# Optimization experiments

Measured on AMD Instinct MI355X. Metric: run time of the kernel, lower is better.

## Reference

```python
import jax, jax.numpy as jnp
import numpy as np

NEG_SLOPE = 0.2  # PyG GATConv default negative_slope


def setup_inputs() -> dict:
    key = jax.random.key(0)
    k_x, k_e, k_w, k_as, k_ad = jax.random.split(key, 5)
    B, F, N, D, E, L = 2, 16, 5000, 128, 40000, 3
    x = jax.random.normal(k_x, (B, F, N, D), dtype=jnp.float32)
    edge_index = jax.random.randint(k_e, (B, F, 2, E), 0, N, dtype=jnp.int64)
    Ws = jax.random.normal(k_w, (L, D, D), dtype=jnp.float32) / np.float32(np.sqrt(D))
    att_src = jax.random.normal(k_as, (L, D), dtype=jnp.float32) / np.float32(np.sqrt(D))
    att_dst = jax.random.normal(k_ad, (L, D), dtype=jnp.float32) / np.float32(np.sqrt(D))
    bias = jnp.zeros((L, D), dtype=jnp.float32)
    return {"x": x, "edge_index": edge_index, "Ws": Ws,
            "att_src": att_src, "att_dst": att_dst, "bias": bias}


def _gat_layer(h, src, dst, n, W, a_s, a_d, b):
    # h: [n, D] node features; src/dst: [E_tot] edge endpoints (self-loops included)
    h2 = h @ W                                   # [n, D] transformed features
    s = h2 @ a_s                                 # [n] per-node source score
    d = h2 @ a_d                                 # [n] per-node dest score
    e = jax.nn.leaky_relu(s[src] + d[dst], NEG_SLOPE)   # [E_tot] raw attention
    m = jax.lax.stop_gradient(jax.ops.segment_max(e, dst, num_segments=n))
    ex = jnp.exp(e - m[dst])                     # numerically stable softmax per dst
    denom = jax.ops.segment_sum(ex, dst, num_segments=n)
    alpha = ex / denom[dst]                      # [E_tot] normalized attention
    out = jax.ops.segment_sum(alpha[:, None] * h2[src], dst, num_segments=n) + b
    return jax.nn.relu(out)


def reference(x, edge_index, Ws, att_src, att_dst, bias):
    B, F, N, D = x.shape
    n = B * F * N
    h = x.reshape(n, D)
    # faithful to torch: (BF,2,E).view(2,-1) is a raw row-major reshape
    ei = edge_index.reshape(2, -1)
    loop = jnp.arange(n, dtype=ei.dtype)         # PyG GATConv adds self-loops
    src = jnp.concatenate([ei[0], loop])
    dst = jnp.concatenate([ei[1], loop])
    for l in range(Ws.shape[0]):                 # fixed small layer loop
        h = _gat_layer(h, src, dst, n, Ws[l], att_src[l], att_dst[l], bias[l])
    return h.reshape(B, F, N, D)
```

## Files before the change

### kernel.cpp

```cpp
#include <hip/hip_runtime.h>
#include <math.h>

#define NODES_TOTAL 160000
#define NODES_REAL  5000
#define D 128
#define NEG 0.2f
#define KP2 128
#define HL2 (128 * KP2)
#define WT2_L (2 * HL2)

typedef unsigned short ushort_t;
typedef unsigned int uint_t;
typedef __attribute__((ext_vector_type(8))) __bf16 bf16x8;
typedef __attribute__((ext_vector_type(4))) float f32x4;
union BF8 { bf16x8 v; ushort_t u[8]; };

__device__ __forceinline__ void split2(float x, ushort_t& hi, ushort_t& lo) {
    unsigned u = __float_as_uint(x);
    hi = (ushort_t)(u >> 16);
    float hif = __uint_as_float(u & 0xffff0000u);
    lo = (ushort_t)(__float_as_uint(x - hif) >> 16);
}
__device__ __forceinline__ uint_t encmax(float f) {
    uint_t b = __float_as_uint(f);
    return b ^ ((uint_t)((int)b >> 31) | 0x80000000u);
}
__device__ __forceinline__ float decmax(uint_t u) {
    uint_t b = (u & 0x80000000u) ? (u ^ 0x80000000u) : ~u;
    return __uint_as_float(b);
}

__global__ void zero_kernel(int* counts, uint_t* gmaxu) {
    int i = blockIdx.x * blockDim.x + threadIdx.x;
    if (i < NODES_REAL) counts[i] = 0;
    if (i < 3) gmaxu[i] = 0u;
}

__global__ void rank_kernel(const int* __restrict__ ei, int* __restrict__ counts,
                            ushort_t* __restrict__ rank16, int Eh) {
    int e = blockIdx.x * blockDim.x + threadIdx.x;
    if (e < Eh) {
        int d = ei[Eh + e];
        int r = atomicAdd(&counts[d], 1);
        rank16[e] = (ushort_t)r;
    }
}

__global__ void scan_kernel(const int* __restrict__ counts, int* __restrict__ offs) {
    __shared__ int sd[1024];
    int t = threadIdx.x;
    int pre[5]; int sum = 0;
    #pragma unroll
    for (int u = 0; u < 5; ++u) {
        int idx = t * 5 + u;
        int c = (idx < NODES_REAL) ? counts[idx] : 0;
        pre[u] = sum; sum += c;
    }
    sd[t] = sum;
    __syncthreads();
    int run = sum;
    for (int o = 1; o < 1024; o <<= 1) {
        int v = (t >= o) ? sd[t - o] : 0;
        __syncthreads();
        sd[t] += v;
        __syncthreads();
    }
    int excl = sd[t] - run;
    #pragma unroll
    for (int u = 0; u < 5; ++u) {
        int idx = t * 5 + u;
        if (idx < NODES_REAL) offs[idx] = excl + pre[u];
    }
    if (t == 1023) offs[NODES_REAL] = excl + run;
}

__global__ void scatter_det(const int* __restrict__ ei, const int* __restrict__ offs,
                            const ushort_t* __restrict__ rank16, ushort_t* __restrict__ esrc,
                            int Eh) {
    int e = blockIdx.x * blockDim.x + threadIdx.x;
    if (e < Eh) {
        int s = ei[e];
        int d = ei[Eh + e];
        esrc[offs[d] + (int)rank16[e]] = (ushort_t)s;
    }
}

__global__ void wsplit_kernel(const float* __restrict__ Ws, ushort_t* __restrict__ Wm) {
    int l  = blockIdx.x >> 3;
    int n  = (blockIdx.x & 7) * 16 + (threadIdx.x >> 4);
    int c8 = threadIdx.x & 15;
    int k0 = c8 * 8;
    const float* src = Ws + (size_t)l * D * D;
    union { ushort_t u[8]; uint4 v; } hi, lo;
    #pragma unroll
    for (int j = 0; j < 8; ++j) split2(src[(size_t)(k0 + j) * D + n], hi.u[j], lo.u[j]);
    int ct = n >> 4, m16 = n & 15, kc = c8 >> 2, qq = c8 & 3;
    int lane = qq * 16 + m16;
    ushort_t* d2 = Wm + (size_t)l * WT2_L + ((ct * 4 + kc) * 2 + 0) * 512 + lane * 8;
    *(uint4*)d2 = hi.v;
    *(uint4*)(d2 + 512) = lo.v;
}

__global__ __launch_bounds__(256, 2)
void mlp3_kernel(const float* __restrict__ x, const ushort_t* __restrict__ Wm,
                 const float* __restrict__ bs, float* __restrict__ out, int row_base) {
    __shared__ float scr[2][2][16][132];
    int tid = threadIdx.x;
    int w = tid >> 6, lane = tid & 63, q = lane >> 4, m16 = lane & 15;
    int p = w >> 1, h = w & 1;
    int row0 = row_base + blockIdx.x * 64 + p * 32;

    float4 xa[2][4][2];
    #pragma unroll
    for (int rt = 0; rt < 2; ++rt) {
        int r = row0 + rt * 16 + m16;
        if (r > NODES_TOTAL - 1) r = NODES_TOTAL - 1;
        #pragma unroll
        for (int kc = 0; kc < 4; ++kc) {
            const float* gp = x + (size_t)r * D + kc * 32 + q * 8;
            xa[rt][kc][0] = *(const float4*)gp;
            xa[rt][kc][1] = *(const float4*)(gp + 4);
        }
    }

    f32x4 acc[2][4];
    #pragma unroll
    for (int l = 0; l < 3; ++l) {
        const ushort_t* Wml = Wm + (size_t)l * WT2_L;
        if (l > 0) __syncthreads();

        BF8 ahi[2][4], alo[2][4];
        #pragma unroll
        for (int rt = 0; rt < 2; ++rt)
            #pragma unroll
            for (int kc = 0; kc < 4; ++kc) {
                float4 v0, v1;
                if (l == 0) { v0 = xa[rt][kc][0]; v1 = xa[rt][kc][1]; }
                else {
                    const float* sp = &scr[p][rt][m16][kc * 32 + q * 8];
                    v0 = *(const float4*)sp; v1 = *(const float4*)(sp + 4);
                }
                float xv[8] = {v0.x, v0.y, v0.z, v0.w, v1.x, v1.y, v1.z, v1.w};
                #pragma unroll
                for (int j = 0; j < 8; ++j) split2(xv[j], ahi[rt][kc].u[j], alo[rt][kc].u[j]);
            }
        if (l > 0) __syncthreads();

        #pragma unroll
        for (int rt = 0; rt < 2; ++rt)
            #pragma unroll
            for (int ct = 0; ct < 4; ++ct) acc[rt][ct] = (f32x4){0.f, 0.f, 0.f, 0.f};

        #pragma unroll
        for (int ph = 0; ph < 2; ++ph) {
            int kc0 = ph * 2;
            bf16x8 bh[4][2], bl[4][2];
            #pragma unroll
            for (int ct = 0; ct < 4; ++ct)
                #pragma unroll
                for (int dk = 0; dk < 2; ++dk) {
                    const ushort_t* bp = Wml + (((h * 4 + ct) * 4 + (kc0 + dk)) * 2) * 512 + lane * 8;
                    bh[ct][dk] = *(const bf16x8*)bp;
                    bl[ct][dk] = *(const bf16x8*)(bp + 512);
                }
            #pragma unroll
            for (int dk = 0; dk < 2; ++dk)
                #pragma unroll
                for (int ct = 0; ct < 4; ++ct)
                    #pragma unroll
                    for (int rt = 0; rt < 2; ++rt) {
                        acc[rt][ct] = __builtin_amdgcn_mfma_f32_16x16x32_bf16(ahi[rt][kc0 + dk].v, bh[ct][dk], acc[rt][ct], 0, 0, 0);
                        acc[rt][ct] = __builtin_amdgcn_mfma_f32_16x16x32_bf16(ahi[rt][kc0 + dk].v, bl[ct][dk], acc[rt][ct], 0, 0, 0);
                        acc[rt][ct] = __builtin_amdgcn_mfma_f32_16x16x32_bf16(alo[rt][kc0 + dk].v, bh[ct][dk], acc[rt][ct], 0, 0, 0);
                    }
        }
        float bv[4];
        #pragma unroll
        for (int ct = 0; ct < 4; ++ct) bv[ct] = bs[l * D + (h * 4 + ct) * 16 + m16];
        #pragma unroll
        for (int rt = 0; rt < 2; ++rt)
            #pragma unroll
            for (int ct = 0; ct < 4; ++ct)
                #pragma unroll
                for (int reg = 0; reg < 4; ++reg)
                    scr[p][rt][q * 4 + reg][(h * 4 + ct) * 16 + m16] =
                        fmaxf(acc[rt][ct][reg] + bv[ct], 0.f);
    }
    __syncthreads();
    #pragma unroll
    for (int i = 0; i < 8; ++i) {
        int rowl = i * 2 + (lane >> 5);
        int grow = row0 + h * 16 + rowl;
        float4 v = *(const float4*)&scr[p][h][rowl][(lane & 31) * 4];
        if (grow < NODES_TOTAL)
            *(float4*)&out[(size_t)grow * D + (lane & 31) * 4] = v;
    }
}

__global__ __launch_bounds__(64, 2)
void gsmall_kernel(const float* __restrict__ hin, const ushort_t* __restrict__ Wm,
                   const float* __restrict__ a_s, const float* __restrict__ a_d,
                   float* __restrict__ h2, float* __restrict__ sv, float* __restrict__ dv,
                   uint_t* __restrict__ gmaxu) {
    int lane = threadIdx.x & 63, q = lane >> 4, m16 = lane & 15;
    int row0 = blockIdx.x * 16;
    float4 xa[4][2];
    {
        int r = row0 + m16;
        if (r > NODES_REAL - 1) r = NODES_REAL - 1;
        #pragma unroll
        for (int kc = 0; kc < 4; ++kc) {
            const float* gp = hin + (size_t)r * D + kc * 32 + q * 8;
            xa[kc][0] = *(const float4*)gp;
            xa[kc][1] = *(const float4*)(gp + 4);
        }
    }
    f32x4 acc[8];
    #pragma unroll
    for (int ct = 0; ct < 8; ++ct) acc[ct] = (f32x4){0.f, 0.f, 0.f, 0.f};

    #pragma unroll
    for (int kc = 0; kc < 4; ++kc) {
        BF8 ahi, alo;
        {
            float4 v0 = xa[kc][0], v1 = xa[kc][1];
            float xv[8] = {v0.x, v0.y, v0.z, v0.w, v1.x, v1.y, v1.z, v1.w};
            #pragma unroll
            for (int j = 0; j < 8; ++j) split2(xv[j], ahi.u[j], alo.u[j]);
        }
        bf16x8 bh[8], bl[8];
        #pragma unroll
        for (int ct = 0; ct < 8; ++ct) {
            const ushort_t* bp = Wm + ((ct * 4 + kc) * 2) * 512 + lane * 8;
            bh[ct] = *(const bf16x8*)bp;
            bl[ct] = *(const bf16x8*)(bp + 512);
        }
        #pragma unroll
        for (int ct = 0; ct < 8; ++ct) {
            acc[ct] = __builtin_amdgcn_mfma_f32_16x16x32_bf16(ahi.v, bh[ct], acc[ct], 0, 0, 0);
            acc[ct] = __builtin_amdgcn_mfma_f32_16x16x32_bf16(ahi.v, bl[ct], acc[ct], 0, 0, 0);
            acc[ct] = __builtin_amdgcn_mfma_f32_16x16x32_bf16(alo.v, bh[ct], acc[ct], 0, 0, 0);
        }
    }
    #pragma unroll
    for (int reg = 0; reg < 4; ++reg) {
        int grow = row0 + q * 4 + reg;
        if (grow < NODES_REAL) {
            #pragma unroll
            for (int ct = 0; ct < 8; ++ct)
                h2[(size_t)grow * D + ct * 16 + m16] = acc[ct][reg];
        }
    }
    float asv[8], adv[8];
    #pragma unroll
    for (int ct = 0; ct < 8; ++ct) { asv[ct] = a_s[ct * 16 + m16]; adv[ct] = a_d[ct * 16 + m16]; }
    #pragma unroll
    for (int reg = 0; reg < 4; ++reg) {
        float ps = 0.f, pd = 0.f;
        #pragma unroll
        for (int ct = 0; ct < 8; ++ct) {
            float v = acc[ct][reg];
            ps += v * asv[ct]; pd += v * adv[ct];
        }
        #pragma unroll
        for (int o = 1; o < 16; o <<= 1) { ps += __shfl_xor(ps, o); pd += __shfl_xor(pd, o); }
        int grow = row0 + q * 4 + reg;
        if (m16 == 0 && grow < NODES_REAL) {
            sv[grow] = ps; dv[grow] = pd;
            atomicMax(gmaxu, encmax(ps));
        }
    }
}

__global__ __launch_bounds__(256)
void agg_kernel(const float* __restrict__ h2, const float* __restrict__ sv,
                const float* __restrict__ dv, const int* __restrict__ offs,
                const ushort_t* __restrict__ esrc, const float* __restrict__ bias,
                float* __restrict__ out, const uint_t* __restrict__ gmaxu) {
    int w = threadIdx.x >> 6, lane = threadIdx.x & 63;
    int i = blockIdx.x * 4 + w;
    int start = offs[i], end = offs[i + 1];
    float d_i = dv[i];
    float gm = decmax(*gmaxu) + d_i;
    float m = gm > 0.f ? gm : NEG * gm;
    const float2* h2v = (const float2*)h2;
    float ax0 = 0.f, ay0 = 0.f, ax1 = 0.f, ay1 = 0.f;
    float ax2 = 0.f, ay2 = 0.f, ax3 = 0.f, ay3 = 0.f, exs = 0.f;
    for (int base = start; base < end; base += 64) {
        int cnt = min(64, end - base);
        int srci = (lane < cnt) ? (int)esrc[base + lane] : 0;
        float sc = sv[srci] + d_i;
        sc = sc > 0.f ? sc : NEG * sc;
        float ex = (lane < cnt) ? __expf(sc - m) : 0.f;
        exs += ex;
        if (cnt == 64) {
            #pragma unroll 2
            for (int j = 0; j < 64; j += 4) {
                int   s0 = __shfl(srci, j),     s1 = __shfl(srci, j + 1);
                int   s2 = __shfl(srci, j + 2), s3 = __shfl(srci, j + 3);
                float e0 = __shfl(ex, j),       e1 = __shfl(ex, j + 1);
                float e2 = __shfl(ex, j + 2),   e3 = __shfl(ex, j + 3);
                float2 hv0 = h2v[(size_t)s0 * 64 + lane];
                float2 hv1 = h2v[(size_t)s1 * 64 + lane];
                float2 hv2 = h2v[(size_t)s2 * 64 + lane];
                float2 hv3 = h2v[(size_t)s3 * 64 + lane];
                ax0 += e0 * hv0.x; ay0 += e0 * hv0.y;
                ax1 += e1 * hv1.x; ay1 += e1 * hv1.y;
                ax2 += e2 * hv2.x; ay2 += e2 * hv2.y;
                ax3 += e3 * hv3.x; ay3 += e3 * hv3.y;
            }
        } else {
            for (int j = 0; j < cnt; ++j) {
                int   src = __shfl(srci, j);
                float e   = __shfl(ex, j);
                float2 hv = h2v[(size_t)src * 64 + lane];
                ax0 += e * hv.x; ay0 += e * hv.y;
            }
        }
    }
    float ax = (ax0 + ax1) + (ax2 + ax3);
    float ay = (ay0 + ay1) + (ay2 + ay3);
    float scf = sv[i] + d_i; scf = scf > 0.f ? scf : NEG * scf;
    float exf = __expf(scf - m);
    float2 hv = h2v[(size_t)i * 64 + lane];
    ax += exf * hv.x; ay += exf * hv.y;
    #pragma unroll
    for (int o = 1; o < 64; o <<= 1) exs += __shfl_xor(exs, o);
    float rd = 1.f / (exs + exf);
    float2 b2 = *(const float2*)&bias[2 * lane];
    float2 o2 = make_float2(fmaxf(ax * rd + b2.x, 0.f), fmaxf(ay * rd + b2.y, 0.f));
    *(float2*)&out[(size_t)i * D + 2 * lane] = o2;
}

extern "C" void kernel_launch(void* const* d_in, const int* in_sizes, int n_in,
                              void* d_out, int out_size, void* d_ws, size_t ws_size,
                              hipStream_t stream) {
    const float* x   = (const float*)d_in[0];
    const int*   ei  = (const int*)d_in[1];
    const float* Ws  = (const float*)d_in[2];
    const float* as_ = (const float*)d_in[3];
    const float* ad_ = (const float*)d_in[4];
    const float* bs  = (const float*)d_in[5];
    float* out = (float*)d_out;
    int Eh = in_sizes[1] / 2;

    char* ws = (char*)d_ws;
    float*    h2     = (float*)ws;
    float*    bufS   = (float*)(ws + 2560000);
    float*    sv     = (float*)(ws + 5120000);
    float*    dv     = (float*)(ws + 5140000);
    int*      counts = (int*)  (ws + 5160000);
    int*      offs   = (int*)  (ws + 5180000);
    ushort_t* rank16 = (ushort_t*)(ws + 5200016);
    ushort_t* esrc   = (ushort_t*)(ws + 7760016);
    ushort_t* Wm     = (ushort_t*)(ws + 10320016);
    uint_t*   gmaxu  = (uint_t*)(ws + 10528912);

    zero_kernel<<<(NODES_REAL + 255) / 256, 256, 0, stream>>>(counts, gmaxu);
    rank_kernel<<<(Eh + 255) / 256, 256, 0, stream>>>(ei, counts, rank16, Eh);
    scan_kernel<<<1, 1024, 0, stream>>>(counts, offs);
    scatter_det<<<(Eh + 255) / 256, 256, 0, stream>>>(ei, offs, rank16, esrc, Eh);
    wsplit_kernel<<<24, 256, 0, stream>>>(Ws, Wm);

    {
        const int rows = NODES_TOTAL - NODES_REAL;
        const int nb   = (rows + 63) / 64;
        const int nb1  = (nb + 2) / 3;
        int base = NODES_REAL;
        for (int s = 0; s < 3; ++s) {
            int b0 = s * nb1;
            int bn = (s == 2) ? (nb - 2 * nb1) : nb1;
            if (bn <= 0) break;
            mlp3_kernel<<<bn, 256, 0, stream>>>(x, Wm, bs, out, base + b0 * 64);
        }
    }

    for (int l = 0; l < 3; ++l) {
        const float* hin = (l == 0) ? x : bufS;
        float* hout = (l == 2) ? out : bufS;
        gsmall_kernel<<<(NODES_REAL + 15) / 16, 64, 0, stream>>>(
            hin, Wm + (size_t)l * WT2_L, as_ + l * D, ad_ + l * D, h2, sv, dv, gmaxu + l);
        agg_kernel<<<(NODES_REAL + 3) / 4, 256, 0, stream>>>(
            h2, sv, dv, offs, esrc, bs + l * D, hout, gmaxu + l);
    }
}
```

Baseline: 540.3 us.

## Use block-local shared-memory ranking, fold zeroing into wsplit, merge MLP launches

Edge ranking now counts per chunk with shared-memory atomics, then does one global atomic per touched node per chunk to get chunk bases. This cuts contention on global counter atomics. The zero kernel is folded into wsplit, and the three mlp3 launches become one. The agg inner loop is software-pipelined so gathers for the next group of four are issued before the FMAs for the current group. The chunk bases live in the h2 scratch buffer, which is safe only because h2 is written later, and the chunk order of global atomics makes edge ordering within a node nondeterministic.

```diff
diff --git a/kernel.cpp b/kernel.cpp
--- a/kernel.cpp
+++ b/kernel.cpp
@@ -8,6 +8,7 @@
 #define KP2 128
 #define HL2 (128 * KP2)
 #define WT2_L (2 * HL2)
+#define CHUNK 16384
 
 typedef unsigned short ushort_t;
 typedef unsigned int uint_t;
@@ -30,19 +31,48 @@
     return __uint_as_float(b);
 }
 
-__global__ void zero_kernel(int* counts, uint_t* gmaxu) {
-    int i = blockIdx.x * blockDim.x + threadIdx.x;
-    if (i < NODES_REAL) counts[i] = 0;
-    if (i < 3) gmaxu[i] = 0u;
-}
-
-__global__ void rank_kernel(const int* __restrict__ ei, int* __restrict__ counts,
-                            ushort_t* __restrict__ rank16, int Eh) {
-    int e = blockIdx.x * blockDim.x + threadIdx.x;
-    if (e < Eh) {
-        int d = ei[Eh + e];
-        int r = atomicAdd(&counts[d], 1);
-        rank16[e] = (ushort_t)r;
+__global__ void wsplit_kernel(const float* __restrict__ Ws, ushort_t* __restrict__ Wm,
+                              int* __restrict__ counts, uint_t* __restrict__ gmaxu) {
+    int gid = blockIdx.x * 256 + threadIdx.x;
+    if (gid < NODES_REAL) counts[gid] = 0;
+    if (gid < 3) gmaxu[gid] = 0u;
+    int l  = blockIdx.x >> 3;
+    int n  = (blockIdx.x & 7) * 16 + (threadIdx.x >> 4);
+    int c8 = threadIdx.x & 15;
+    int k0 = c8 * 8;
+    const float* src = Ws + (size_t)l * D * D;
+    union { ushort_t u[8]; uint4 v; } hi, lo;
+    #pragma unroll
+    for (int j = 0; j < 8; ++j) split2(src[(size_t)(k0 + j) * D + n], hi.u[j], lo.u[j]);
+    int ct = n >> 4, m16 = n & 15, kc = c8 >> 2, qq = c8 & 3;
+    int lane = qq * 16 + m16;
+    ushort_t* d2 = Wm + (size_t)l * WT2_L + ((ct * 4 + kc) * 2 + 0) * 512 + lane * 8;
+    *(uint4*)d2 = hi.v;
+    *(uint4*)(d2 + 512) = lo.v;
+}
+
+__global__ __launch_bounds__(256)
+void rank2_kernel(const int* __restrict__ ei, int* __restrict__ counts,
+                  int* __restrict__ bases, ushort_t* __restrict__ rank16, int Eh) {
+    __shared__ uint_t lc[NODES_REAL];
+    int c = blockIdx.x, tid = threadIdx.x;
+    for (int i = tid; i < NODES_REAL; i += 256) lc[i] = 0u;
+    __syncthreads();
+    int e0 = c * CHUNK;
+    #pragma unroll 4
+    for (int k = 0; k < CHUNK / 256; ++k) {
+        int e = e0 + k * 256 + tid;
+        if (e < Eh) {
+            int d = ei[Eh + e];
+            uint_t r = atomicAdd(&lc[d], 1u);
+            rank16[e] = (ushort_t)r;
+        }
+    }
+    __syncthreads();
+    for (int i = tid; i < NODES_REAL; i += 256) {
+        uint_t n = lc[i];
+        if (n > 0u)
+            bases[c * NODES_REAL + i] = atomicAdd(&counts[i], (int)n);
     }
 }
 
@@ -75,40 +105,26 @@
 }
 
 __global__ void scatter_det(const int* __restrict__ ei, const int* __restrict__ offs,
+                            const int* __restrict__ bases,
                             const ushort_t* __restrict__ rank16, ushort_t* __restrict__ esrc,
                             int Eh) {
     int e = blockIdx.x * blockDim.x + threadIdx.x;
     if (e < Eh) {
         int s = ei[e];
         int d = ei[Eh + e];
-        esrc[offs[d] + (int)rank16[e]] = (ushort_t)s;
-    }
-}
-
-__global__ void wsplit_kernel(const float* __restrict__ Ws, ushort_t* __restrict__ Wm) {
-    int l  = blockIdx.x >> 3;
-    int n  = (blockIdx.x & 7) * 16 + (threadIdx.x >> 4);
-    int c8 = threadIdx.x & 15;
-    int k0 = c8 * 8;
-    const float* src = Ws + (size_t)l * D * D;
-    union { ushort_t u[8]; uint4 v; } hi, lo;
-    #pragma unroll
-    for (int j = 0; j < 8; ++j) split2(src[(size_t)(k0 + j) * D + n], hi.u[j], lo.u[j]);
-    int ct = n >> 4, m16 = n & 15, kc = c8 >> 2, qq = c8 & 3;
-    int lane = qq * 16 + m16;
-    ushort_t* d2 = Wm + (size_t)l * WT2_L + ((ct * 4 + kc) * 2 + 0) * 512 + lane * 8;
-    *(uint4*)d2 = hi.v;
-    *(uint4*)(d2 + 512) = lo.v;
+        int c = e >> 14;
+        esrc[offs[d] + bases[c * NODES_REAL + d] + (int)rank16[e]] = (ushort_t)s;
+    }
 }
 
 __global__ __launch_bounds__(256, 2)
 void mlp3_kernel(const float* __restrict__ x, const ushort_t* __restrict__ Wm,
-                 const float* __restrict__ bs, float* __restrict__ out, int row_base) {
+                 const float* __restrict__ bs, float* __restrict__ out) {
     __shared__ float scr[2][2][16][132];
     int tid = threadIdx.x;
     int w = tid >> 6, lane = tid & 63, q = lane >> 4, m16 = lane & 15;
     int p = w >> 1, h = w & 1;
-    int row0 = row_base + blockIdx.x * 64 + p * 32;
+    int row0 = NODES_REAL + blockIdx.x * 64 + p * 32;
 
     float4 xa[2][4][2];
     #pragma unroll
@@ -294,21 +310,30 @@
         float ex = (lane < cnt) ? __expf(sc - m) : 0.f;
         exs += ex;
         if (cnt == 64) {
-            #pragma unroll 2
-            for (int j = 0; j < 64; j += 4) {
-                int   s0 = __shfl(srci, j),     s1 = __shfl(srci, j + 1);
-                int   s2 = __shfl(srci, j + 2), s3 = __shfl(srci, j + 3);
-                float e0 = __shfl(ex, j),       e1 = __shfl(ex, j + 1);
-                float e2 = __shfl(ex, j + 2),   e3 = __shfl(ex, j + 3);
-                float2 hv0 = h2v[(size_t)s0 * 64 + lane];
-                float2 hv1 = h2v[(size_t)s1 * 64 + lane];
-                float2 hv2 = h2v[(size_t)s2 * 64 + lane];
-                float2 hv3 = h2v[(size_t)s3 * 64 + lane];
+            float e0 = __shfl(ex, 0), e1 = __shfl(ex, 1);
+            float e2 = __shfl(ex, 2), e3 = __shfl(ex, 3);
+            float2 hv0 = h2v[(size_t)__shfl(srci, 0) * 64 + lane];
+            float2 hv1 = h2v[(size_t)__shfl(srci, 1) * 64 + lane];
+            float2 hv2 = h2v[(size_t)__shfl(srci, 2) * 64 + lane];
+            float2 hv3 = h2v[(size_t)__shfl(srci, 3) * 64 + lane];
+            for (int j = 4; j < 64; j += 4) {
+                float f0 = __shfl(ex, j),     f1 = __shfl(ex, j + 1);
+                float f2 = __shfl(ex, j + 2), f3 = __shfl(ex, j + 3);
+                float2 nv0 = h2v[(size_t)__shfl(srci, j) * 64 + lane];
+                float2 nv1 = h2v[(size_t)__shfl(srci, j + 1) * 64 + lane];
+                float2 nv2 = h2v[(size_t)__shfl(srci, j + 2) * 64 + lane];
+                float2 nv3 = h2v[(size_t)__shfl(srci, j + 3) * 64 + lane];
                 ax0 += e0 * hv0.x; ay0 += e0 * hv0.y;
                 ax1 += e1 * hv1.x; ay1 += e1 * hv1.y;
                 ax2 += e2 * hv2.x; ay2 += e2 * hv2.y;
                 ax3 += e3 * hv3.x; ay3 += e3 * hv3.y;
+                e0 = f0; e1 = f1; e2 = f2; e3 = f3;
+                hv0 = nv0; hv1 = nv1; hv2 = nv2; hv3 = nv3;
             }
+            ax0 += e0 * hv0.x; ay0 += e0 * hv0.y;
+            ax1 += e1 * hv1.x; ay1 += e1 * hv1.y;
+            ax2 += e2 * hv2.x; ay2 += e2 * hv2.y;
+            ax3 += e3 * hv3.x; ay3 += e3 * hv3.y;
         } else {
             for (int j = 0; j < cnt; ++j) {
                 int   src = __shfl(srci, j);
@@ -343,6 +368,7 @@
     const float* bs  = (const float*)d_in[5];
     float* out = (float*)d_out;
     int Eh = in_sizes[1] / 2;
+    int nchunks = (Eh + CHUNK - 1) / CHUNK;
 
     char* ws = (char*)d_ws;
     float*    h2     = (float*)ws;
@@ -355,25 +381,14 @@
     ushort_t* esrc   = (ushort_t*)(ws + 7760016);
     ushort_t* Wm     = (ushort_t*)(ws + 10320016);
     uint_t*   gmaxu  = (uint_t*)(ws + 10528912);
-
-    zero_kernel<<<(NODES_REAL + 255) / 256, 256, 0, stream>>>(counts, gmaxu);
-    rank_kernel<<<(Eh + 255) / 256, 256, 0, stream>>>(ei, counts, rank16, Eh);
+    int*      bases  = (int*)h2;
+
+    wsplit_kernel<<<24, 256, 0, stream>>>(Ws, Wm, counts, gmaxu);
+    rank2_kernel<<<nchunks, 256, 0, stream>>>(ei, counts, bases, rank16, Eh);
     scan_kernel<<<1, 1024, 0, stream>>>(counts, offs);
-    scatter_det<<<(Eh + 255) / 256, 256, 0, stream>>>(ei, offs, rank16, esrc, Eh);
-    wsplit_kernel<<<24, 256, 0, stream>>>(Ws, Wm);
-
-    {
-        const int rows = NODES_TOTAL - NODES_REAL;
-        const int nb   = (rows + 63) / 64;
-        const int nb1  = (nb + 2) / 3;
-        int base = NODES_REAL;
-        for (int s = 0; s < 3; ++s) {
-            int b0 = s * nb1;
-            int bn = (s == 2) ? (nb - 2 * nb1) : nb1;
-            if (bn <= 0) break;
-            mlp3_kernel<<<bn, 256, 0, stream>>>(x, Wm, bs, out, base + b0 * 64);
-        }
-    }
+    scatter_det<<<(Eh + 255) / 256, 256, 0, stream>>>(ei, offs, bases, rank16, esrc, Eh);
+
+    mlp3_kernel<<<(NODES_TOTAL - NODES_REAL + 63) / 64, 256, 0, stream>>>(x, Wm, bs, out);
 
     for (int l = 0; l < 3; ++l) {
         const float* hin = (l == 0) ? x : bufS;
```

Result: faster. 487.9 us (-9.7%).
